# Kernel tuning notes

Measured on AMD Instinct MI355X. Metric: run time of the kernel, lower is better.

Reference implementation:

```python
import jax, jax.numpy as jnp
import numpy as np

# Physical constants and grid (match torch WRF.__init__)
PREF = 100000.0
RD = 287.0
G = 9.81
NX, NY, NZ = 384, 384, 48
DX, DY = 1000.0, 1000.0
DZ = 1.0 / (NZ + 1)

# --- staggered-grid stencil primitives (replace F.conv3d with shifts) ---

def pad_x(X):
    # periodic in x
    return jnp.concatenate([X[:, :, -1:], X, X[:, :, :1]], axis=2)

def pad_y(X):
    # periodic in y
    return jnp.concatenate([X[:, -1:, :], X, X[:, :1, :]], axis=1)

def pad_z(X, top=None, surface=None):
    # Dirichlet in z (defaults to zero boundary planes)
    top = top if top is not None else jnp.zeros_like(X[:1])
    surface = surface if surface is not None else jnp.zeros_like(X[:1])
    return jnp.concatenate([top, X, surface], axis=0)

def bar_x(X):
    return (X[:, :, 1:] + X[:, :, :-1]) * 0.5

def bar_y(X):
    return (X[:, 1:, :] + X[:, :-1, :]) * 0.5

def bar_z(X):
    return (X[1:] + X[:-1]) * 0.5

def delta_x(X):
    return (X[:, :, 1:] - X[:, :, :-1]) / DX

def delta_y(X):
    return (X[:, 1:, :] - X[:, :-1, :]) / DY

def delta_z(X):
    return (X[1:] - X[:-1]) / DZ


def rhs(U, V, W, Theta, Mu, Phi, Phi_t, Phi_s, P_t, P_s):
    u = U / bar_x(pad_x(Mu))                      # (NZ, NY, NX+1)
    v = V / bar_y(pad_y(Mu))                      # (NZ, NY+1, NX)
    w = W / bar_z(Mu)                             # (NZ-1, NY, NX)
    alpha = -delta_z(pad_z(Phi, Phi_t, Phi_s)) / Mu   # (NZ, NY, NX)
    theta = Theta / Mu
    p = PREF * (RD * theta / PREF / alpha) ** 1.4
    omega = -w * G / bar_z(alpha) / bar_z(Mu)     # (NZ-1, NY, NX)
    Omega = omega * bar_z(Mu)

    R_U = (-delta_x(bar_x(pad_x(U)) * bar_x(pad_x(u)))
           - delta_y(bar_x(pad_x(V)) * bar_y(pad_y(u)))
           - delta_z(bar_x(pad_x(pad_z(Omega))) * bar_z(pad_z(u))))
    R_V = (-delta_x(bar_y(pad_y(U)) * bar_x(pad_x(v)))
           - delta_y(bar_y(pad_y(V)) * bar_y(pad_y(v)))
           - delta_z(bar_y(pad_y(pad_z(Omega))) * bar_z(pad_z(v))))
    R_W = (-delta_x(bar_z(U) * bar_x(pad_x(w)))
           - delta_y(bar_z(V) * bar_y(pad_y(w)))
           - delta_z(bar_z(pad_z(Omega)) * bar_z(pad_z(w))))
    R_Theta = (-delta_x(U * bar_x(pad_x(theta)))
               - delta_y(V * bar_y(pad_y(theta)))
               - delta_z(pad_z(Omega) * bar_z(pad_z(theta))))
    R_Phi = (-bar_z(bar_x(u)) * delta_x(bar_x(pad_x(Phi)))
             - bar_z(bar_y(v)) * delta_y(bar_y(pad_y(Phi)))
             - omega * delta_z(bar_z(pad_z(Phi, Phi_t, Phi_s))))
    R_Mu = -delta_x(U) - delta_y(V) - delta_z(pad_z(Omega))

    # pressure-gradient terms
    R_U = R_U + (-bar_x(pad_x(Mu)) * bar_x(pad_x(alpha)) * delta_x(pad_x(p))
                 - delta_z(bar_x(bar_z(pad_x(pad_z(p, P_t, P_s)))))
                   * delta_x(pad_x(bar_z(pad_z(Phi, Phi_t, Phi_s)))))
    R_V = R_V + (-bar_y(pad_y(Mu)) * bar_y(pad_y(alpha)) * delta_y(pad_y(p))
                 - delta_z(bar_y(bar_z(pad_y(pad_z(p, P_t, P_s)))))
                   * delta_y(pad_y(bar_z(pad_z(Phi, Phi_t, Phi_s)))))
    R_W = R_W + G * (delta_z(p) - bar_z(Mu))
    R_Phi = R_Phi + G * w
    return R_U, R_V, R_W, R_Theta, R_Mu, R_Phi


def rk3_step(U, V, W, Theta, Mu, Phi, Phi_t, Phi_s, P_t, P_s, dt):
    Uc, Vc, Wc, Tc, Mc, Pc = U, V, W, Theta, Mu, Phi
    for c in (dt / 3.0, dt / 2.0, dt * 1.0):
        rU, rV, rW, rT, rM, rP = rhs(Uc, Vc, Wc, Tc, Mc, Pc, Phi_t, Phi_s, P_t, P_s)
        Uc = U + c * rU
        Vc = V + c * rV
        Wc = W + c * rW
        Tc = Theta + c * rT
        Mc = Mu + c * rM
        Pc = Phi + c * rP
    return (Uc, Vc, Wc, Tc, Mc, Pc)


def setup_inputs() -> dict:
    key = jax.random.key(0)
    k_th, k_u, k_v, k_w = jax.random.split(key, 4)
    # potential temperature with boundary layers, ~300 K
    theta_full = 300.0 + 0.5 * jax.random.normal(k_th, (NZ + 2, NY, NX), dtype=jnp.float32)
    P_t = jnp.zeros((1, NY, NX), dtype=jnp.float32)
    P_s = jnp.full((1, NY, NX), PREF, dtype=jnp.float32)
    # reproduce __init__ hydrostatic setup
    P = jnp.linspace(DZ, 1.0 - DZ, NZ, dtype=jnp.float32).reshape(NZ, 1, 1) * (P_s - P_t) + P_t
    Alpha = RD / PREF * theta_full[1:-1] * (P / PREF) ** (-1.0 / 1.4)
    Mu = jnp.broadcast_to(P_s - P_t, (NZ, NY, NX)).astype(jnp.float32)
    layer = Mu * Alpha * DZ                                  # (NZ, NY, NX)
    # Phi_full[i] = sum_{j>=i} layer[j], Phi_full[NZ] = 0
    Phi_full = jnp.concatenate(
        [jnp.flip(jnp.cumsum(jnp.flip(layer, 0), axis=0), 0),
         jnp.zeros((1, NY, NX), dtype=jnp.float32)], axis=0)  # (NZ+1, NY, NX)
    Phi_t = Phi_full[:1]
    Phi_s = Phi_full[-1:]
    Phi = Phi_full[1:-1]                                     # (NZ-1, NY, NX)
    Theta = theta_full[1:-1] * Mu
    U = 5e5 * jax.random.normal(k_u, (NZ, NY, NX + 1), dtype=jnp.float32)
    V = 5e5 * jax.random.normal(k_v, (NZ, NY + 1, NX), dtype=jnp.float32)
    W = 1e4 * jax.random.normal(k_w, (NZ - 1, NY, NX), dtype=jnp.float32)
    return {"U": U, "V": V, "W": W, "Theta": Theta, "Mu": Mu, "Phi": Phi,
            "Phi_t": Phi_t, "Phi_s": Phi_s, "P_t": P_t, "P_s": P_s, "dt": 4}


def reference(U, V, W, Theta, Mu, Phi, Phi_t, Phi_s, P_t, P_s, dt):
    return rk3_step(U, V, W, Theta, Mu, Phi, Phi_t, Phi_s, P_t, P_s, dt)
```

## Files before the change

kernel.cpp:

```cpp
#include <hip/hip_runtime.h>

namespace {

constexpr int NX = 384, NY = 384, NZ = 48;
constexpr int NXU = NX + 1;
constexpr int PLN = NX * NY;
constexpr float RDX = 1.0f / 1000.0f;
constexpr float RDY = 1.0f / 1000.0f;
constexpr float RDZ = 49.0f;
constexpr float PREF = 100000.0f, G = 9.81f;
constexpr float K_RP = 287.0f / PREF;

constexpr int SZ_U = NZ * NY * NXU;
constexpr int SZ_V = NZ * (NY + 1) * NX;
constexpr int SZ_W = (NZ - 1) * PLN;
constexpr int SZ_T = NZ * PLN;
constexpr int SZ_M = NZ * PLN;
constexpr int SZ_P = (NZ - 1) * PLN;

constexpr int TX = 32, TY = 8;
constexpr int PW = TX + 3;
constexpr int PH = TY + 3;
constexpr int PSZ = PW * PH;
constexpr int WW = PW + 1;
constexpr int WH = PH + 1;
constexpr int WSZ = WW * WH;
constexpr int ZP = 448;
constexpr int KCH = 12, KSPLIT = 4;

constexpr int O_PH = 0;
constexpr int O_MS = O_PH + 5 * ZP;
constexpr int O_UR = O_MS + 4 * ZP;
constexpr int O_VR = O_UR + 3 * ZP;
constexpr int O_TS = O_VR + 3 * ZP;
constexpr int O_WS = O_TS + ZP;
constexpr int O_P  = O_WS + ZP;
constexpr int O_OM = O_P  + 3 * PSZ;
constexpr int O_TH = O_OM + 3 * PSZ;
constexpr int O_u  = O_TH + 2 * PSZ;
constexpr int O_v  = O_u  + 2 * PSZ;
constexpr int O_w  = O_v  + 2 * PSZ;
constexpr int LTOT = O_w + 2 * PSZ;

__device__ __forceinline__ float frcp(float x) { return __builtin_amdgcn_rcpf(x); }
__device__ __forceinline__ float pow14(float x) {
    return __builtin_amdgcn_exp2f(1.4f * __builtin_amdgcn_logf(x));
}
__device__ __forceinline__ void gll4(const float* src, float* ldsWaveBase) {
    __builtin_amdgcn_global_load_lds(
        (const __attribute__((address_space(1))) void*)src,
        (__attribute__((address_space(3))) void*)ldsWaveBase, 4, 0, 0);
}
__device__ __forceinline__ int imin(int a, int b) { return a < b ? a : b; }
__device__ __forceinline__ int imax(int a, int b) { return a > b ? a : b; }

__global__ __launch_bounds__(256, 3)
void rhs_tile(
    const float* __restrict__ Us, const float* __restrict__ Vs, const float* __restrict__ Ws,
    const float* __restrict__ Ts, const float* __restrict__ Ms, const float* __restrict__ Ps,
    const float* __restrict__ Phit, const float* __restrict__ Phis,
    const float* __restrict__ Pt,   const float* __restrict__ Psrf,
    const float* __restrict__ U0, const float* __restrict__ V0, const float* __restrict__ W0,
    const float* __restrict__ T0, const float* __restrict__ M0, const float* __restrict__ P0,
    float* __restrict__ Uo, float* __restrict__ Vo, float* __restrict__ Wo,
    float* __restrict__ To, float* __restrict__ Mo, float* __restrict__ Po,
    const int* __restrict__ dtp, float coef)
{
    __shared__ float L[LTOT];

    const int tx = threadIdx.x, ty = threadIdx.y;
    const int tid = ty * TX + tx;
    const int i0 = blockIdx.x * TX;
    const int j0 = blockIdx.y * TY;
    const int k0 = blockIdx.z * KCH;
    const int i = i0 + tx, j = j0 + ty;
    const float c = coef * (float)(*dtp);
    const int ly = ty + 1, lx = tx + 1;
    const int wb = tid & ~63;
    const bool w2 = (tid < 192);
    const bool has2 = (tid + 256 < PSZ);

    auto mkcell = [&](int idx, int& pix, int& uo, int& vo) {
        const int r = idx / PW, cc = idx - r * PW;
        int gj = j0 - 1 + r;  if (gj < 0) gj += NY; else if (gj >= NY) gj -= NY;
        int gi = i0 - 1 + cc; if (gi < 0) gi += NX; else if (gi >= NX) gi -= NX;
        int gII = i0 - 1 + cc; if (gII < 0) gII += NX + 1; else if (gII > NX) gII -= NX + 1;
        int gJJ = j0 - 1 + r;  if (gJJ < 0) gJJ += NY + 1; else if (gJJ > NY) gJJ -= NY + 1;
        pix = gj * NX + gi; uo = gj * NXU + gII; vo = gJJ * NX + gi;
    };
    auto mkwide = [&](int idxw, int& pixw) {
        const int r = idxw / WW, cc = idxw - r * WW;
        int gj = j0 - 2 + r;  if (gj < 0) gj += NY; else if (gj >= NY) gj -= NY;
        int gi = i0 - 2 + cc; if (gi < 0) gi += NX; else if (gi >= NX) gi -= NX;
        pixw = gj * NX + gi;
    };
    int pixA, uoA, voA, pixB, uoB, voB, pwA, pwB;
    mkcell(tid, pixA, uoA, voA);
    mkcell(imin(tid + 256, PSZ - 1), pixB, uoB, voB);
    mkwide(tid, pwA);
    mkwide(imin(tid + 256, WSZ - 1), pwB);

    auto stage = [&](int k) {
        {
            const int m = k + 3;
            const float* sA = (m >= NZ - 1) ? &Phis[pixA] : &Ps[m * PLN + pixA];
            gll4(sA, &L[O_PH + (m % 5) * ZP + wb]);
            if (w2) {
                const float* sB = (m >= NZ - 1) ? &Phis[pixB] : &Ps[m * PLN + pixB];
                gll4(sB, &L[O_PH + (m % 5) * ZP + wb + 256]);
            }
        }
        {
            const int lc = imin(k + 3, NZ - 1);
            gll4(&Ms[lc * PLN + pwA], &L[O_MS + ((k + 3) % 4) * ZP + wb]);
            if (w2) gll4(&Ms[lc * PLN + pwB], &L[O_MS + ((k + 3) % 4) * ZP + wb + 256]);
        }
        {
            const int lc = imin(k + 2, NZ - 1);
            gll4(&Us[lc * NY * NXU + uoA], &L[O_UR + ((k + 2) % 3) * ZP + wb]);
            if (w2) gll4(&Us[lc * NY * NXU + uoB], &L[O_UR + ((k + 2) % 3) * ZP + wb + 256]);
            gll4(&Vs[lc * (NY + 1) * NX + voA], &L[O_VR + ((k + 2) % 3) * ZP + wb]);
            if (w2) gll4(&Vs[lc * (NY + 1) * NX + voB], &L[O_VR + ((k + 2) % 3) * ZP + wb + 256]);
            gll4(&Ts[lc * PLN + pixA], &L[O_TS + wb]);
            if (w2) gll4(&Ts[lc * PLN + pixB], &L[O_TS + wb + 256]);
            const int lw = imin(k + 2, NZ - 2);
            gll4(&Ws[lw * PLN + pixA], &L[O_WS + wb]);
            if (w2) gll4(&Ws[lw * PLN + pixB], &L[O_WS + wb + 256]);
        }
    };

    auto derive = [&](int l, int idx, int pix, float tsv, float wsv) {
        const int r = idx / PW, cc = idx - r * PW;
        const int wc = (r + 1) * WW + (cc + 1);
        const int s3 = ((l % 3) + 3) % 3, s2 = l & 1;
        float pv, th = 0.f, uv = 0.f, vv = 0.f, wv = 0.f, om = 0.f;
        if (l >= 0 && l < NZ) {
            const int m4 = l % 4, m5 = l % 5, p5 = ((l - 1) % 5 + 5) % 5;
            const float mu  = L[O_MS + m4 * ZP + wc];
            const float phv = L[O_PH + m5 * ZP + idx];
            const float phm = L[O_PH + p5 * ZP + idx];
            const float rmu = frcp(mu);
            const float al  = -(phv - phm) * RDZ * rmu;
            th = tsv * rmu;
            pv = PREF * pow14(K_RP * th * frcp(al));
            uv = L[O_UR + (l % 3) * ZP + idx]
                 * frcp(0.5f * (L[O_MS + m4 * ZP + wc - 1] + L[O_MS + m4 * ZP + wc]));
            vv = L[O_VR + (l % 3) * ZP + idx]
                 * frcp(0.5f * (L[O_MS + m4 * ZP + wc - WW] + L[O_MS + m4 * ZP + wc]));
            if (l < NZ - 1) {
                const float mu1 = L[O_MS + ((l + 1) % 4) * ZP + wc];
                const float ph1 = L[O_PH + ((l + 1) % 5) * ZP + idx];
                const float al1 = -(ph1 - phv) * RDZ * frcp(mu1);
                const float mz  = 0.5f * (mu + mu1);
                wv = wsv * frcp(mz);
                om = -wsv * G * frcp(0.5f * (al + al1) * mz);
            }
        } else {
            pv = (l < 0) ? Pt[pix] : Psrf[pix];
        }
        L[O_P  + s3 * PSZ + idx] = pv;
        L[O_OM + s3 * PSZ + idx] = om;
        L[O_TH + s2 * PSZ + idx] = th;
        L[O_u  + s2 * PSZ + idx] = uv;
        L[O_v  + s2 * PSZ + idx] = vv;
        L[O_w  + s2 * PSZ + idx] = wv;
    };

    {
        auto fillDirect = [&](int idx, int pix, int uo, int vo, int pixw, bool doW) {
            for (int m = k0 - 2; m <= k0 + 2; ++m) {
                float v = (m >= NZ - 1) ? Phis[pix] : ((m < 0) ? Phit[pix] : Ps[m * PLN + pix]);
                L[O_PH + ((m % 5 + 5) % 5) * ZP + idx] = v;
            }
            if (doW) {
                for (int l = k0 - 1; l <= k0 + 2; ++l) {
                    const int lc = imin(imax(l, 0), NZ - 1);
                    L[O_MS + ((l % 4 + 4) % 4) * ZP + pixw == pixw ? 0 : 0];
                }
            }
            (void)uo; (void)vo;
        };
        (void)fillDirect;
        for (int m = k0 - 2; m <= k0 + 2; ++m) {
            float v = (m >= NZ - 1) ? Phis[pixA] : ((m < 0) ? Phit[pixA] : Ps[m * PLN + pixA]);
            L[O_PH + ((m % 5 + 5) % 5) * ZP + tid] = v;
        }
        for (int l = k0 - 1; l <= k0 + 2; ++l) {
            const int lc = imin(imax(l, 0), NZ - 1);
            L[O_MS + ((l % 4 + 4) % 4) * ZP + tid] = Ms[lc * PLN + pwA];
        }
        for (int l = k0 - 1; l <= k0 + 1; ++l) {
            const int lc = imin(imax(l, 0), NZ - 1);
            L[O_UR + ((l % 3 + 3) % 3) * ZP + tid] = Us[lc * NY * NXU + uoA];
            L[O_VR + ((l % 3 + 3) % 3) * ZP + tid] = Vs[lc * (NY + 1) * NX + voA];
        }
        if (has2) {
            const int idx = tid + 256;
            for (int m = k0 - 2; m <= k0 + 2; ++m) {
                float v = (m >= NZ - 1) ? Phis[pixB] : ((m < 0) ? Phit[pixB] : Ps[m * PLN + pixB]);
                L[O_PH + ((m % 5 + 5) % 5) * ZP + idx] = v;
            }
            for (int l = k0 - 1; l <= k0 + 1; ++l) {
                const int lc = imin(imax(l, 0), NZ - 1);
                L[O_UR + ((l % 3 + 3) % 3) * ZP + idx] = Us[lc * NY * NXU + uoB];
                L[O_VR + ((l % 3 + 3) % 3) * ZP + idx] = Vs[lc * (NY + 1) * NX + voB];
            }
        }
        if (tid + 256 < WSZ) {
            const int idx = tid + 256;
            for (int l = k0 - 1; l <= k0 + 2; ++l) {
                const int lc = imin(imax(l, 0), NZ - 1);
                L[O_MS + ((l % 4 + 4) % 4) * ZP + idx] = Ms[lc * PLN + pwB];
            }
        }
    }
    __syncthreads();

    {
        int lc = imin(imax(k0 - 1, 0), NZ - 1), lw = imin(imax(k0 - 1, 0), NZ - 2);
        derive(k0 - 1, tid, pixA, Ts[lc * PLN + pixA], Ws[lw * PLN + pixA]);
        if (has2) derive(k0 - 1, tid + 256, pixB, Ts[lc * PLN + pixB], Ws[lw * PLN + pixB]);
        lc = imin(k0, NZ - 1); lw = imin(k0, NZ - 2);
        derive(k0, tid, pixA, Ts[lc * PLN + pixA], Ws[lw * PLN + pixA]);
        if (has2) derive(k0, tid + 256, pixB, Ts[lc * PLN + pixB], Ws[lw * PLN + pixB]);
    }
    {
        const int lc = imin(k0 + 1, NZ - 1), lw = imin(k0 + 1, NZ - 2);
        gll4(&Ts[lc * PLN + pixA], &L[O_TS + wb]);
        if (w2) gll4(&Ts[lc * PLN + pixB], &L[O_TS + wb + 256]);
        gll4(&Ws[lw * PLN + pixA], &L[O_WS + wb]);
        if (w2) gll4(&Ws[lw * PLN + pixB], &L[O_WS + wb + 256]);
    }
    __syncthreads();

    const int e0 = (k0 - 1) & 1;
    float th_m  = L[O_TH + e0 * PSZ + ly * PW + lx];
    float u_m   = L[O_u  + e0 * PSZ + ly * PW + lx];
    float u_m_e = L[O_u  + e0 * PSZ + ly * PW + lx + 1];
    float v_m   = L[O_v  + e0 * PSZ + (ly + 1) * PW + lx - PW + PW];
    float v_m_  = L[O_v  + e0 * PSZ + ly * PW + lx];
    float v_m_e = L[O_v  + e0 * PSZ + (ly + 1) * PW + lx];
    float w_m   = L[O_w  + e0 * PSZ + ly * PW + lx];
    v_m = v_m_;

    for (int k = k0; k < k0 + KCH; ++k) {
        derive(k + 1, tid, pixA, L[O_TS + tid], L[O_WS + tid]);
        if (has2) derive(k + 1, tid + 256, pixB, L[O_TS + tid + 256], L[O_WS + tid + 256]);
        __syncthreads();

        stage(k);

        const int a5 = (k + 4) % 5, b5 = k % 5, c5 = (k + 1) % 5;
        const int aP = (k + 2) % 3, bP = k % 3, cP = (k + 1) % 3;
        const int m4 = k % 4, n4 = (k + 1) % 4;
        const int e = k & 1, f = 1 - e;
        const int eU = k % 3, fU = (k + 1) % 3;

        auto PHx = [&](int s, int rr, int cc) { return L[O_PH + s * ZP + rr * PW + cc]; };
        auto Px  = [&](int s, int rr, int cc) { return L[O_P  + s * PSZ + rr * PW + cc]; };
        auto Ox  = [&](int s, int rr, int cc) { return L[O_OM + s * PSZ + rr * PW + cc]; };
        auto MUx = [&](int s, int rr, int cc) { return L[O_MS + s * ZP + (rr + 1) * WW + cc + 1]; };
        auto THx = [&](int s, int rr, int cc) { return L[O_TH + s * PSZ + rr * PW + cc]; };
        auto URx = [&](int s, int rr, int cc) { return L[O_UR + s * ZP + rr * PW + cc]; };
        auto VRx = [&](int s, int rr, int cc) { return L[O_VR + s * ZP + rr * PW + cc]; };
        auto ux  = [&](int s, int rr, int cc) { return L[O_u  + s * PSZ + rr * PW + cc]; };
        auto vx  = [&](int s, int rr, int cc) { return L[O_v  + s * PSZ + rr * PW + cc]; };
        auto wx  = [&](int s, int rr, int cc) { return L[O_w  + s * PSZ + rr * PW + cc]; };
        auto ALk = [&](int rr, int cc) {
            return -(PHx(b5, rr, cc) - PHx(a5, rr, cc)) * RDZ * frcp(MUx(m4, rr, cc));
        };

        auto R_U_c = [&](int cc, float ukm) -> float {
            const float u0 = ux(e, ly, cc), um = ux(e, ly, cc - 1), up = ux(e, ly, cc + 1);
            const float Uc = URx(eU, ly, cc), Um = URx(eU, ly, cc - 1), Up = URx(eU, ly, cc + 1);
            float r = -0.25f * ((Uc + Up) * (u0 + up) - (Um + Uc) * (um + u0)) * RDX;
            const float VBj  = 0.5f * (VRx(eU, ly, cc - 1) + VRx(eU, ly, cc));
            const float VBj1 = 0.5f * (VRx(eU, ly + 1, cc - 1) + VRx(eU, ly + 1, cc));
            const float uS = ux(e, ly - 1, cc), uN = ux(e, ly + 1, cc);
            r -= (VBj1 * 0.5f * (u0 + uN) - VBj * 0.5f * (uS + u0)) * RDY;
            const float OBk  = 0.5f * (Ox(aP, ly, cc - 1) + Ox(aP, ly, cc));
            const float OBk1 = 0.5f * (Ox(bP, ly, cc - 1) + Ox(bP, ly, cc));
            const float ukp = ux(f, ly, cc);
            r -= (OBk1 * 0.5f * (u0 + ukp) - OBk * 0.5f * (ukm + u0)) * RDZ;
            const float mux_ = 0.5f * (MUx(m4, ly, cc - 1) + MUx(m4, ly, cc));
            const float alx  = 0.5f * (ALk(ly, cc - 1) + ALk(ly, cc));
            const float dpx  = (Px(bP, ly, cc) - Px(bP, ly, cc - 1)) * RDX;
            r -= mux_ * alx * dpx;
            const float pzk  = 0.25f * (Px(aP, ly, cc - 1) + Px(bP, ly, cc - 1)
                                      + Px(aP, ly, cc)     + Px(bP, ly, cc));
            const float pzk1 = 0.25f * (Px(bP, ly, cc - 1) + Px(cP, ly, cc - 1)
                                      + Px(bP, ly, cc)     + Px(cP, ly, cc));
            const float dpz = (pzk1 - pzk) * RDZ;
            const float pza = 0.5f * (PHx(a5, ly, cc - 1) + PHx(b5, ly, cc - 1));
            const float pzb = 0.5f * (PHx(a5, ly, cc)     + PHx(b5, ly, cc));
            r -= dpz * (pzb - pza) * RDX;
            return r;
        };

        auto R_V_c = [&](int rr, float vkm) -> float {
            const float v0 = vx(e, rr, lx), vm = vx(e, rr - 1, lx), vp = vx(e, rr + 1, lx);
            const float Vc = VRx(eU, rr, lx), Vm = VRx(eU, rr - 1, lx), Vp = VRx(eU, rr + 1, lx);
            float r = -0.25f * ((Vc + Vp) * (v0 + vp) - (Vm + Vc) * (vm + v0)) * RDY;
            const float UBi  = 0.5f * (URx(eU, rr - 1, lx)     + URx(eU, rr, lx));
            const float UBi1 = 0.5f * (URx(eU, rr - 1, lx + 1) + URx(eU, rr, lx + 1));
            const float vW = vx(e, rr, lx - 1), vE = vx(e, rr, lx + 1);
            r -= (UBi1 * 0.5f * (v0 + vE) - UBi * 0.5f * (vW + v0)) * RDX;
            const float OBk  = 0.5f * (Ox(aP, rr - 1, lx) + Ox(aP, rr, lx));
            const float OBk1 = 0.5f * (Ox(bP, rr - 1, lx) + Ox(bP, rr, lx));
            const float vkp = vx(f, rr, lx);
            r -= (OBk1 * 0.5f * (v0 + vkp) - OBk * 0.5f * (vkm + v0)) * RDZ;
            const float muy = 0.5f * (MUx(m4, rr - 1, lx) + MUx(m4, rr, lx));
            const float aly = 0.5f * (ALk(rr - 1, lx) + ALk(rr, lx));
            const float dpy = (Px(bP, rr, lx) - Px(bP, rr - 1, lx)) * RDY;
            r -= muy * aly * dpy;
            const float pzk  = 0.25f * (Px(aP, rr - 1, lx) + Px(bP, rr - 1, lx)
                                      + Px(aP, rr, lx)     + Px(bP, rr, lx));
            const float pzk1 = 0.25f * (Px(bP, rr - 1, lx) + Px(cP, rr - 1, lx)
                                      + Px(bP, rr, lx)     + Px(cP, rr, lx));
            const float dpz = (pzk1 - pzk) * RDZ;
            const float pza = 0.5f * (PHx(a5, rr - 1, lx) + PHx(b5, rr - 1, lx));
            const float pzb = 0.5f * (PHx(a5, rr, lx)     + PHx(b5, rr, lx));
            r -= dpz * (pzb - pza) * RDY;
            return r;
        };

        const float th0 = THx(e, ly, lx);
        float rT = -(URx(eU, ly, lx + 1) * 0.5f * (th0 + THx(e, ly, lx + 1))
                   - URx(eU, ly, lx)     * 0.5f * (THx(e, ly, lx - 1) + th0)) * RDX
                   -(VRx(eU, ly + 1, lx) * 0.5f * (th0 + THx(e, ly + 1, lx))
                   - VRx(eU, ly, lx)     * 0.5f * (THx(e, ly - 1, lx) + th0)) * RDY;
        const float th_p = THx(f, ly, lx);
        const float Hk  = Ox(aP, ly, lx) * 0.5f * (th_m + th0);
        const float Hk1 = Ox(bP, ly, lx) * 0.5f * (th0 + th_p);
        rT -= (Hk1 - Hk) * RDZ;

        const float rM = -(URx(eU, ly, lx + 1) - URx(eU, ly, lx)) * RDX
                         -(VRx(eU, ly + 1, lx) - VRx(eU, ly, lx)) * RDY
                         -(Ox(bP, ly, lx) - Ox(aP, ly, lx)) * RDZ;

        const int idc = (k * NY + j) * NX + i;
        To[idc] = T0[idc] + c * rT;
        Mo[idc] = M0[idc] + c * rM;
        const int idu = (k * NY + j) * NXU + i;
        Uo[idu] = U0[idu] + c * R_U_c(lx, u_m);
        const int idv = (k * (NY + 1) + j) * NX + i;
        Vo[idv] = V0[idv] + c * R_V_c(ly, v_m);

        if (k < NZ - 1) {
            const float w0 = wx(e, ly, lx);
            const float Uzi  = 0.5f * (URx(eU, ly, lx)     + URx(fU, ly, lx));
            const float Uzi1 = 0.5f * (URx(eU, ly, lx + 1) + URx(fU, ly, lx + 1));
            const float wW = wx(e, ly, lx - 1), wE = wx(e, ly, lx + 1);
            float rW = -(Uzi1 * 0.5f * (w0 + wE) - Uzi * 0.5f * (wW + w0)) * RDX;
            const float Vzj  = 0.5f * (VRx(eU, ly, lx)     + VRx(fU, ly, lx));
            const float Vzj1 = 0.5f * (VRx(eU, ly + 1, lx) + VRx(fU, ly + 1, lx));
            const float wS = wx(e, ly - 1, lx), wN = wx(e, ly + 1, lx);
            rW -= (Vzj1 * 0.5f * (w0 + wN) - Vzj * 0.5f * (wS + w0)) * RDY;
            const float OZk  = 0.5f * (Ox(aP, ly, lx) + Ox(bP, ly, lx));
            const float OZk1 = 0.5f * (Ox(bP, ly, lx) + Ox(cP, ly, lx));
            const float wkp = wx(f, ly, lx);
            rW -= (OZk1 * 0.5f * (w0 + wkp) - OZk * 0.5f * (w_m + w0)) * RDZ;
            const float muz = 0.5f * (MUx(m4, ly, lx) + MUx(n4, ly, lx));
            rW += G * ((Px(cP, ly, lx) - Px(bP, ly, lx)) * RDZ - muz);

            const float ubz = 0.25f * (ux(e, ly, lx) + ux(e, ly, lx + 1)
                                     + ux(f, ly, lx) + ux(f, ly, lx + 1));
            const float dfx = (PHx(b5, ly, lx + 1) - PHx(b5, ly, lx - 1)) * (0.5f * RDX);
            const float vbz = 0.25f * (vx(e, ly, lx) + vx(e, ly + 1, lx)
                                     + vx(f, ly, lx) + vx(f, ly + 1, lx));
            const float dfy = (PHx(b5, ly + 1, lx) - PHx(b5, ly - 1, lx)) * (0.5f * RDY);
            const float rmuz = frcp(muz);
            const float om   = Ox(bP, ly, lx) * rmuz;
            const float dfz  = (PHx(c5, ly, lx) - PHx(a5, ly, lx)) * (0.5f * RDZ);
            const float rP = -ubz * dfx - vbz * dfy - om * dfz + G * w0;

            Wo[idc] = W0[idc] + c * rW;
            Po[idc] = P0[idc] + c * rP;
        }

        if (i == NX - 1) {
            Uo[idu + 1] = U0[idu + 1] + c * R_U_c(lx + 1, u_m_e);
        }
        if (j == NY - 1) {
            const int idv2 = (k * (NY + 1) + NY) * NX + i;
            Vo[idv2] = V0[idv2] + c * R_V_c(ly + 1, v_m_e);
        }

        th_m  = th0;
        u_m   = ux(e, ly, lx);
        u_m_e = ux(e, ly, lx + 1);
        v_m   = vx(e, ly, lx);
        v_m_e = vx(e, ly + 1, lx);
        w_m   = wx(e, ly, lx);

        __syncthreads();
    }
}

}

extern "C" void kernel_launch(void* const* d_in, const int* in_sizes, int n_in,
                              void* d_out, int out_size, void* d_ws, size_t ws_size,
                              hipStream_t stream)
{
    (void)in_sizes; (void)n_in; (void)out_size; (void)ws_size;

    const float* U0   = (const float*)d_in[0];
    const float* V0   = (const float*)d_in[1];
    const float* W0   = (const float*)d_in[2];
    const float* T0   = (const float*)d_in[3];
    const float* M0   = (const float*)d_in[4];
    const float* P0   = (const float*)d_in[5];
    const float* Phit = (const float*)d_in[6];
    const float* Phis = (const float*)d_in[7];
    const float* Pt   = (const float*)d_in[8];
    const float* Psrf = (const float*)d_in[9];
    const int*   dtp  = (const int*)d_in[10];

    float* out = (float*)d_out;
    float* ws  = (float*)d_ws;

    float* outU = out;
    float* outV = outU + SZ_U;
    float* outW = outV + SZ_V;
    float* outT = outW + SZ_W;
    float* outM = outT + SZ_T;
    float* outP = outM + SZ_M;

    float* wsU = ws;
    float* wsV = wsU + SZ_U;
    float* wsW = wsV + SZ_V;
    float* wsT = wsW + SZ_W;
    float* wsM = wsT + SZ_T;
    float* wsP = wsM + SZ_M;

    const dim3 blk(TX, TY, 1);
    const dim3 grd(NX / TX, NY / TY, KSPLIT);

    const float coefs[3] = {1.0f / 3.0f, 0.5f, 1.0f};

    const float* sU[3] = {U0, outU, wsU};
    const float* sV[3] = {V0, outV, wsV};
    const float* sW[3] = {W0, outW, wsW};
    const float* sT[3] = {T0, outT, wsT};
    const float* sM[3] = {M0, outM, wsM};
    const float* sP_[3] = {P0, outP, wsP};
    float* oU[3] = {outU, wsU, outU};
    float* oV[3] = {outV, wsV, outV};
    float* oW[3] = {outW, wsW, outW};
    float* oT[3] = {outT, wsT, outT};
    float* oM[3] = {outM, wsM, outM};
    float* oP[3] = {outP, wsP, outP};

    for (int s = 0; s < 3; ++s) {
        rhs_tile<<<grd, blk, 0, stream>>>(
            sU[s], sV[s], sW[s], sT[s], sM[s], sP_[s],
            Phit, Phis, Pt, Psrf,
            U0, V0, W0, T0, M0, P0,
            oU[s], oV[s], oW[s], oT[s], oM[s], oP[s],
            dtp, coefs[s]);
    }
}
```

Measured before the change: 606.8 us.

## Switch to 16x16 tiles with a one-cell halo and tighter LDS layout

Changes the thread tile from 32x8 to 16x16 and shrinks the halo from 3 to 2 cells, so the LDS footprint per block drops and occupancy is raised to 4 blocks per CU. Halo cells past the async-load range are staged with scalar loads in a tail path, and the east/north edge faces now fetch the wrapped U/V value directly from global memory instead of relying on the wider halo. The aim is less redundant halo traffic and more resident waves. The cost is more boundary special-casing, extra scalar loads, and a square tile that may coalesce less well along x.

After: 715.6 us. 1.18x slower.

```diff
diff --git a/kernel.cpp b/kernel.cpp
--- a/kernel.cpp
+++ b/kernel.cpp
@@ -18,29 +18,29 @@
 constexpr int SZ_M = NZ * PLN;
 constexpr int SZ_P = (NZ - 1) * PLN;
 
-constexpr int TX = 32, TY = 8;
-constexpr int PW = TX + 3;
-constexpr int PH = TY + 3;
+constexpr int TX = 16, TY = 16;
+constexpr int PW = TX + 2;
+constexpr int PH = TY + 2;
 constexpr int PSZ = PW * PH;
 constexpr int WW = PW + 1;
-constexpr int WH = PH + 1;
-constexpr int WSZ = WW * WH;
-constexpr int ZP = 448;
+constexpr int WSZ = WW * WW;
 constexpr int KCH = 12, KSPLIT = 4;
 
 constexpr int O_PH = 0;
-constexpr int O_MS = O_PH + 5 * ZP;
-constexpr int O_UR = O_MS + 4 * ZP;
-constexpr int O_VR = O_UR + 3 * ZP;
-constexpr int O_TS = O_VR + 3 * ZP;
-constexpr int O_WS = O_TS + ZP;
-constexpr int O_P  = O_WS + ZP;
+constexpr int O_MS = O_PH + 5 * PSZ;
+constexpr int O_UR = O_MS + 4 * WSZ;
+constexpr int O_VR = O_UR + 3 * PSZ;
+constexpr int O_TS = O_VR + 3 * PSZ;
+constexpr int O_WS = O_TS + PSZ;
+constexpr int O_P  = O_WS + PSZ;
 constexpr int O_OM = O_P  + 3 * PSZ;
 constexpr int O_TH = O_OM + 3 * PSZ;
 constexpr int O_u  = O_TH + 2 * PSZ;
 constexpr int O_v  = O_u  + 2 * PSZ;
 constexpr int O_w  = O_v  + 2 * PSZ;
 constexpr int LTOT = O_w + 2 * PSZ;
+
+struct PIdx { int pix, uo, vo, wc, oxa, oxb, oya, oyb; };
 
 __device__ __forceinline__ float frcp(float x) { return __builtin_amdgcn_rcpf(x); }
 __device__ __forceinline__ float pow14(float x) {
@@ -54,7 +54,7 @@
 __device__ __forceinline__ int imin(int a, int b) { return a < b ? a : b; }
 __device__ __forceinline__ int imax(int a, int b) { return a > b ? a : b; }
 
-__global__ __launch_bounds__(256, 3)
+__global__ __launch_bounds__(256, 4)
 void rhs_tile(
     const float* __restrict__ Us, const float* __restrict__ Vs, const float* __restrict__ Ws,
     const float* __restrict__ Ts, const float* __restrict__ Ms, const float* __restrict__ Ps,
@@ -77,86 +77,118 @@
     const float c = coef * (float)(*dtp);
     const int ly = ty + 1, lx = tx + 1;
     const int wb = tid & ~63;
-    const bool w2 = (tid < 192);
-    const bool has2 = (tid + 256 < PSZ);
-
-    auto mkcell = [&](int idx, int& pix, int& uo, int& vo) {
+    const bool hasB = (tid + 256 < PSZ);
+    const bool hasW = (tid + 256 < WSZ);
+
+    auto mkpt = [&](int idx, PIdx& q) {
         const int r = idx / PW, cc = idx - r * PW;
         int gj = j0 - 1 + r;  if (gj < 0) gj += NY; else if (gj >= NY) gj -= NY;
         int gi = i0 - 1 + cc; if (gi < 0) gi += NX; else if (gi >= NX) gi -= NX;
-        int gII = i0 - 1 + cc; if (gII < 0) gII += NX + 1; else if (gII > NX) gII -= NX + 1;
-        int gJJ = j0 - 1 + r;  if (gJJ < 0) gJJ += NY + 1; else if (gJJ > NY) gJJ -= NY + 1;
-        pix = gj * NX + gi; uo = gj * NXU + gII; vo = gJJ * NX + gi;
+        int gII = i0 - 1 + cc; if (gII < 0) gII += NX + 1;
+        int gJJ = j0 - 1 + r;  if (gJJ < 0) gJJ += NY + 1;
+        q.pix = gj * NX + gi;
+        q.uo  = gj * NXU + gII;
+        q.vo  = gJJ * NX + gi;
+        q.wc  = (r + 1) * WW + (cc + 1);
+        q.oxa = q.wc - 1; q.oxb = q.wc;
+        if (i0 == 0 && cc == 0) { q.oxa = q.wc; q.oxb = q.wc + 1; }
+        q.oya = q.wc - WW; q.oyb = q.wc;
+        if (j0 == 0 && r == 0)  { q.oya = q.wc; q.oyb = q.wc + WW; }
     };
-    auto mkwide = [&](int idxw, int& pixw) {
+    auto mkwide = [&](int idxw) -> int {
         const int r = idxw / WW, cc = idxw - r * WW;
         int gj = j0 - 2 + r;  if (gj < 0) gj += NY; else if (gj >= NY) gj -= NY;
         int gi = i0 - 2 + cc; if (gi < 0) gi += NX; else if (gi >= NX) gi -= NX;
-        pixw = gj * NX + gi;
+        return gj * NX + gi;
     };
-    int pixA, uoA, voA, pixB, uoB, voB, pwA, pwB;
-    mkcell(tid, pixA, uoA, voA);
-    mkcell(imin(tid + 256, PSZ - 1), pixB, uoB, voB);
-    mkwide(tid, pwA);
-    mkwide(imin(tid + 256, WSZ - 1), pwB);
+    PIdx A, B;
+    mkpt(tid, A);
+    mkpt(imin(tid + 256, PSZ - 1), B);
+    const int pwA = mkwide(tid);
+    const int pwB = mkwide(imin(tid + 256, WSZ - 1));
+
+    const int tpi = tid - 64;
+    const bool hasTail  = (tpi >= 0 && tpi < PSZ - 320);
+    const int twi = tid - 68;
+    const bool hasWTail = (twi >= 0 && twi < WSZ - 320);
+    PIdx Tq;
+    mkpt(hasTail ? (320 + tpi) : 0, Tq);
+    const int pwT = mkwide(hasWTail ? (320 + twi) : 0);
 
     auto stage = [&](int k) {
         {
             const int m = k + 3;
-            const float* sA = (m >= NZ - 1) ? &Phis[pixA] : &Ps[m * PLN + pixA];
-            gll4(sA, &L[O_PH + (m % 5) * ZP + wb]);
-            if (w2) {
-                const float* sB = (m >= NZ - 1) ? &Phis[pixB] : &Ps[m * PLN + pixB];
-                gll4(sB, &L[O_PH + (m % 5) * ZP + wb + 256]);
+            const float* sA = (m >= NZ - 1) ? &Phis[A.pix] : &Ps[m * PLN + A.pix];
+            gll4(sA, &L[O_PH + (m % 5) * PSZ + wb]);
+            if (tid < 64) {
+                const float* sB = (m >= NZ - 1) ? &Phis[B.pix] : &Ps[m * PLN + B.pix];
+                gll4(sB, &L[O_PH + (m % 5) * PSZ + wb + 256]);
             }
         }
         {
-            const int lc = imin(k + 3, NZ - 1);
-            gll4(&Ms[lc * PLN + pwA], &L[O_MS + ((k + 3) % 4) * ZP + wb]);
-            if (w2) gll4(&Ms[lc * PLN + pwB], &L[O_MS + ((k + 3) % 4) * ZP + wb + 256]);
+            const int lm = imin(k + 3, NZ - 1);
+            gll4(&Ms[lm * PLN + pwA], &L[O_MS + ((k + 3) % 4) * WSZ + wb]);
+            if (tid < 64) gll4(&Ms[lm * PLN + pwB], &L[O_MS + ((k + 3) % 4) * WSZ + wb + 256]);
         }
         {
             const int lc = imin(k + 2, NZ - 1);
-            gll4(&Us[lc * NY * NXU + uoA], &L[O_UR + ((k + 2) % 3) * ZP + wb]);
-            if (w2) gll4(&Us[lc * NY * NXU + uoB], &L[O_UR + ((k + 2) % 3) * ZP + wb + 256]);
-            gll4(&Vs[lc * (NY + 1) * NX + voA], &L[O_VR + ((k + 2) % 3) * ZP + wb]);
-            if (w2) gll4(&Vs[lc * (NY + 1) * NX + voB], &L[O_VR + ((k + 2) % 3) * ZP + wb + 256]);
-            gll4(&Ts[lc * PLN + pixA], &L[O_TS + wb]);
-            if (w2) gll4(&Ts[lc * PLN + pixB], &L[O_TS + wb + 256]);
+            gll4(&Us[lc * NY * NXU + A.uo], &L[O_UR + ((k + 2) % 3) * PSZ + wb]);
+            if (tid < 64) gll4(&Us[lc * NY * NXU + B.uo], &L[O_UR + ((k + 2) % 3) * PSZ + wb + 256]);
+            gll4(&Vs[lc * (NY + 1) * NX + A.vo], &L[O_VR + ((k + 2) % 3) * PSZ + wb]);
+            if (tid < 64) gll4(&Vs[lc * (NY + 1) * NX + B.vo], &L[O_VR + ((k + 2) % 3) * PSZ + wb + 256]);
+            gll4(&Ts[lc * PLN + A.pix], &L[O_TS + wb]);
+            if (tid < 64) gll4(&Ts[lc * PLN + B.pix], &L[O_TS + wb + 256]);
             const int lw = imin(k + 2, NZ - 2);
-            gll4(&Ws[lw * PLN + pixA], &L[O_WS + wb]);
-            if (w2) gll4(&Ws[lw * PLN + pixB], &L[O_WS + wb + 256]);
+            gll4(&Ws[lw * PLN + A.pix], &L[O_WS + wb]);
+            if (tid < 64) gll4(&Ws[lw * PLN + B.pix], &L[O_WS + wb + 256]);
         }
     };
 
-    auto derive = [&](int l, int idx, int pix, float tsv, float wsv) {
-        const int r = idx / PW, cc = idx - r * PW;
-        const int wc = (r + 1) * WW + (cc + 1);
+    auto stage_tail = [&](int k) {
+        if (hasTail) {
+            const int idx = 320 + tpi;
+            const int m = k + 3;
+            L[O_PH + (m % 5) * PSZ + idx] =
+                (m >= NZ - 1) ? Phis[Tq.pix] : Ps[m * PLN + Tq.pix];
+            const int lc = imin(k + 2, NZ - 1);
+            L[O_UR + ((k + 2) % 3) * PSZ + idx] = Us[lc * NY * NXU + Tq.uo];
+            L[O_VR + ((k + 2) % 3) * PSZ + idx] = Vs[lc * (NY + 1) * NX + Tq.vo];
+            L[O_TS + idx] = Ts[lc * PLN + Tq.pix];
+            const int lw = imin(k + 2, NZ - 2);
+            L[O_WS + idx] = Ws[lw * PLN + Tq.pix];
+        }
+        if (hasWTail) {
+            const int lm = imin(k + 3, NZ - 1);
+            L[O_MS + ((k + 3) % 4) * WSZ + 320 + twi] = Ms[lm * PLN + pwT];
+        }
+    };
+
+    auto derive = [&](int l, int idx, const PIdx& q, float tsv, float wsv) {
         const int s3 = ((l % 3) + 3) % 3, s2 = l & 1;
         float pv, th = 0.f, uv = 0.f, vv = 0.f, wv = 0.f, om = 0.f;
         if (l >= 0 && l < NZ) {
             const int m4 = l % 4, m5 = l % 5, p5 = ((l - 1) % 5 + 5) % 5;
-            const float mu  = L[O_MS + m4 * ZP + wc];
-            const float phv = L[O_PH + m5 * ZP + idx];
-            const float phm = L[O_PH + p5 * ZP + idx];
+            const float mu  = L[O_MS + m4 * WSZ + q.wc];
+            const float phv = L[O_PH + m5 * PSZ + idx];
+            const float phm = L[O_PH + p5 * PSZ + idx];
             const float rmu = frcp(mu);
             const float al  = -(phv - phm) * RDZ * rmu;
             th = tsv * rmu;
             pv = PREF * pow14(K_RP * th * frcp(al));
-            uv = L[O_UR + (l % 3) * ZP + idx]
-                 * frcp(0.5f * (L[O_MS + m4 * ZP + wc - 1] + L[O_MS + m4 * ZP + wc]));
-            vv = L[O_VR + (l % 3) * ZP + idx]
-                 * frcp(0.5f * (L[O_MS + m4 * ZP + wc - WW] + L[O_MS + m4 * ZP + wc]));
+            uv = L[O_UR + (l % 3) * PSZ + idx]
+                 * frcp(0.5f * (L[O_MS + m4 * WSZ + q.oxa] + L[O_MS + m4 * WSZ + q.oxb]));
+            vv = L[O_VR + (l % 3) * PSZ + idx]
+                 * frcp(0.5f * (L[O_MS + m4 * WSZ + q.oya] + L[O_MS + m4 * WSZ + q.oyb]));
             if (l < NZ - 1) {
-                const float mu1 = L[O_MS + ((l + 1) % 4) * ZP + wc];
-                const float ph1 = L[O_PH + ((l + 1) % 5) * ZP + idx];
+                const float mu1 = L[O_MS + ((l + 1) % 4) * WSZ + q.wc];
+                const float ph1 = L[O_PH + ((l + 1) % 5) * PSZ + idx];
                 const float al1 = -(ph1 - phv) * RDZ * frcp(mu1);
                 const float mz  = 0.5f * (mu + mu1);
                 wv = wsv * frcp(mz);
                 om = -wsv * G * frcp(0.5f * (al + al1) * mz);
             }
         } else {
-            pv = (l < 0) ? Pt[pix] : Psrf[pix];
+            pv = (l < 0) ? Pt[q.pix] : Psrf[q.pix];
         }
         L[O_P  + s3 * PSZ + idx] = pv;
         L[O_OM + s3 * PSZ + idx] = om;
@@ -167,50 +199,38 @@
     };
 
     {
-        auto fillDirect = [&](int idx, int pix, int uo, int vo, int pixw, bool doW) {
-            for (int m = k0 - 2; m <= k0 + 2; ++m) {
-                float v = (m >= NZ - 1) ? Phis[pix] : ((m < 0) ? Phit[pix] : Ps[m * PLN + pix]);
-                L[O_PH + ((m % 5 + 5) % 5) * ZP + idx] = v;
-            }
-            if (doW) {
-                for (int l = k0 - 1; l <= k0 + 2; ++l) {
-                    const int lc = imin(imax(l, 0), NZ - 1);
-                    L[O_MS + ((l % 4 + 4) % 4) * ZP + pixw == pixw ? 0 : 0];
-                }
-            }
-            (void)uo; (void)vo;
-        };
-        (void)fillDirect;
         for (int m = k0 - 2; m <= k0 + 2; ++m) {
-            float v = (m >= NZ - 1) ? Phis[pixA] : ((m < 0) ? Phit[pixA] : Ps[m * PLN + pixA]);
-            L[O_PH + ((m % 5 + 5) % 5) * ZP + tid] = v;
+            const float v = (m >= NZ - 1) ? Phis[A.pix]
+                          : ((m < 0) ? Phit[A.pix] : Ps[m * PLN + A.pix]);
+            L[O_PH + ((m % 5 + 5) % 5) * PSZ + tid] = v;
         }
         for (int l = k0 - 1; l <= k0 + 2; ++l) {
             const int lc = imin(imax(l, 0), NZ - 1);
-            L[O_MS + ((l % 4 + 4) % 4) * ZP + tid] = Ms[lc * PLN + pwA];
+            L[O_MS + ((l % 4 + 4) % 4) * WSZ + tid] = Ms[lc * PLN + pwA];
         }
         for (int l = k0 - 1; l <= k0 + 1; ++l) {
             const int lc = imin(imax(l, 0), NZ - 1);
-            L[O_UR + ((l % 3 + 3) % 3) * ZP + tid] = Us[lc * NY * NXU + uoA];
-            L[O_VR + ((l % 3 + 3) % 3) * ZP + tid] = Vs[lc * (NY + 1) * NX + voA];
-        }
-        if (has2) {
+            L[O_UR + ((l % 3 + 3) % 3) * PSZ + tid] = Us[lc * NY * NXU + A.uo];
+            L[O_VR + ((l % 3 + 3) % 3) * PSZ + tid] = Vs[lc * (NY + 1) * NX + A.vo];
+        }
+        if (hasB) {
             const int idx = tid + 256;
             for (int m = k0 - 2; m <= k0 + 2; ++m) {
-                float v = (m >= NZ - 1) ? Phis[pixB] : ((m < 0) ? Phit[pixB] : Ps[m * PLN + pixB]);
-                L[O_PH + ((m % 5 + 5) % 5) * ZP + idx] = v;
+                const float v = (m >= NZ - 1) ? Phis[B.pix]
+                              : ((m < 0) ? Phit[B.pix] : Ps[m * PLN + B.pix]);
+                L[O_PH + ((m % 5 + 5) % 5) * PSZ + idx] = v;
             }
             for (int l = k0 - 1; l <= k0 + 1; ++l) {
                 const int lc = imin(imax(l, 0), NZ - 1);
-                L[O_UR + ((l % 3 + 3) % 3) * ZP + idx] = Us[lc * NY * NXU + uoB];
-                L[O_VR + ((l % 3 + 3) % 3) * ZP + idx] = Vs[lc * (NY + 1) * NX + voB];
+                L[O_UR + ((l % 3 + 3) % 3) * PSZ + idx] = Us[lc * NY * NXU + B.uo];
+                L[O_VR + ((l % 3 + 3) % 3) * PSZ + idx] = Vs[lc * (NY + 1) * NX + B.vo];
             }
         }
-        if (tid + 256 < WSZ) {
+        if (hasW) {
             const int idx = tid + 256;
             for (int l = k0 - 1; l <= k0 + 2; ++l) {
                 const int lc = imin(imax(l, 0), NZ - 1);
-                L[O_MS + ((l % 4 + 4) % 4) * ZP + idx] = Ms[lc * PLN + pwB];
+                L[O_MS + ((l % 4 + 4) % 4) * WSZ + idx] = Ms[lc * PLN + pwB];
             }
         }
     }
@@ -218,18 +238,22 @@
 
     {
         int lc = imin(imax(k0 - 1, 0), NZ - 1), lw = imin(imax(k0 - 1, 0), NZ - 2);
-        derive(k0 - 1, tid, pixA, Ts[lc * PLN + pixA], Ws[lw * PLN + pixA]);
-        if (has2) derive(k0 - 1, tid + 256, pixB, Ts[lc * PLN + pixB], Ws[lw * PLN + pixB]);
+        derive(k0 - 1, tid, A, Ts[lc * PLN + A.pix], Ws[lw * PLN + A.pix]);
+        if (hasB) derive(k0 - 1, tid + 256, B, Ts[lc * PLN + B.pix], Ws[lw * PLN + B.pix]);
         lc = imin(k0, NZ - 1); lw = imin(k0, NZ - 2);
-        derive(k0, tid, pixA, Ts[lc * PLN + pixA], Ws[lw * PLN + pixA]);
-        if (has2) derive(k0, tid + 256, pixB, Ts[lc * PLN + pixB], Ws[lw * PLN + pixB]);
+        derive(k0, tid, A, Ts[lc * PLN + A.pix], Ws[lw * PLN + A.pix]);
+        if (hasB) derive(k0, tid + 256, B, Ts[lc * PLN + B.pix], Ws[lw * PLN + B.pix]);
     }
     {
         const int lc = imin(k0 + 1, NZ - 1), lw = imin(k0 + 1, NZ - 2);
-        gll4(&Ts[lc * PLN + pixA], &L[O_TS + wb]);
-        if (w2) gll4(&Ts[lc * PLN + pixB], &L[O_TS + wb + 256]);
-        gll4(&Ws[lw * PLN + pixA], &L[O_WS + wb]);
-        if (w2) gll4(&Ws[lw * PLN + pixB], &L[O_WS + wb + 256]);
+        gll4(&Ts[lc * PLN + A.pix], &L[O_TS + wb]);
+        if (tid < 64) gll4(&Ts[lc * PLN + B.pix], &L[O_TS + wb + 256]);
+        gll4(&Ws[lw * PLN + A.pix], &L[O_WS + wb]);
+        if (tid < 64) gll4(&Ws[lw * PLN + B.pix], &L[O_WS + wb + 256]);
+        if (hasTail) {
+            L[O_TS + 320 + tpi] = Ts[lc * PLN + Tq.pix];
+            L[O_WS + 320 + tpi] = Ws[lw * PLN + Tq.pix];
+        }
     }
     __syncthreads();
 
@@ -237,15 +261,14 @@
     float th_m  = L[O_TH + e0 * PSZ + ly * PW + lx];
     float u_m   = L[O_u  + e0 * PSZ + ly * PW + lx];
     float u_m_e = L[O_u  + e0 * PSZ + ly * PW + lx + 1];
-    float v_m   = L[O_v  + e0 * PSZ + (ly + 1) * PW + lx - PW + PW];
-    float v_m_  = L[O_v  + e0 * PSZ + ly * PW + lx];
+    float v_m   = L[O_v  + e0 * PSZ + ly * PW + lx];
     float v_m_e = L[O_v  + e0 * PSZ + (ly + 1) * PW + lx];
     float w_m   = L[O_w  + e0 * PSZ + ly * PW + lx];
-    v_m = v_m_;
 
     for (int k = k0; k < k0 + KCH; ++k) {
-        derive(k + 1, tid, pixA, L[O_TS + tid], L[O_WS + tid]);
-        if (has2) derive(k + 1, tid + 256, pixB, L[O_TS + tid + 256], L[O_WS + tid + 256]);
+        derive(k + 1, tid, A, L[O_TS + tid], L[O_WS + tid]);
+        if (hasB) derive(k + 1, tid + 256, B, L[O_TS + tid + 256], L[O_WS + tid + 256]);
+        stage_tail(k);
         __syncthreads();
 
         stage(k);
@@ -256,13 +279,13 @@
         const int e = k & 1, f = 1 - e;
         const int eU = k % 3, fU = (k + 1) % 3;
 
-        auto PHx = [&](int s, int rr, int cc) { return L[O_PH + s * ZP + rr * PW + cc]; };
+        auto PHx = [&](int s, int rr, int cc) { return L[O_PH + s * PSZ + rr * PW + cc]; };
         auto Px  = [&](int s, int rr, int cc) { return L[O_P  + s * PSZ + rr * PW + cc]; };
         auto Ox  = [&](int s, int rr, int cc) { return L[O_OM + s * PSZ + rr * PW + cc]; };
-        auto MUx = [&](int s, int rr, int cc) { return L[O_MS + s * ZP + (rr + 1) * WW + cc + 1]; };
+        auto MUx = [&](int s, int rr, int cc) { return L[O_MS + s * WSZ + (rr + 1) * WW + cc + 1]; };
         auto THx = [&](int s, int rr, int cc) { return L[O_TH + s * PSZ + rr * PW + cc]; };
-        auto URx = [&](int s, int rr, int cc) { return L[O_UR + s * ZP + rr * PW + cc]; };
-        auto VRx = [&](int s, int rr, int cc) { return L[O_VR + s * ZP + rr * PW + cc]; };
+        auto URx = [&](int s, int rr, int cc) { return L[O_UR + s * PSZ + rr * PW + cc]; };
+        auto VRx = [&](int s, int rr, int cc) { return L[O_VR + s * PSZ + rr * PW + cc]; };
         auto ux  = [&](int s, int rr, int cc) { return L[O_u  + s * PSZ + rr * PW + cc]; };
         auto vx  = [&](int s, int rr, int cc) { return L[O_v  + s * PSZ + rr * PW + cc]; };
         auto wx  = [&](int s, int rr, int cc) { return L[O_w  + s * PSZ + rr * PW + cc]; };
@@ -270,9 +293,12 @@
             return -(PHx(b5, rr, cc) - PHx(a5, rr, cc)) * RDZ * frcp(MUx(m4, rr, cc));
         };
 
-        auto R_U_c = [&](int cc, float ukm) -> float {
-            const float u0 = ux(e, ly, cc), um = ux(e, ly, cc - 1), up = ux(e, ly, cc + 1);
-            const float Uc = URx(eU, ly, cc), Um = URx(eU, ly, cc - 1), Up = URx(eU, ly, cc + 1);
+        auto R_U_c = [&](int cc, float ukm, float Upov, bool edge) -> float {
+            const float u0 = ux(e, ly, cc), um = ux(e, ly, cc - 1);
+            const float up = edge ? Upov * frcp(0.5f * (MUx(m4, ly, PW - 2) + MUx(m4, ly, PW - 1)))
+                                  : ux(e, ly, cc + 1);
+            const float Uc = URx(eU, ly, cc), Um = URx(eU, ly, cc - 1);
+            const float Up = edge ? Upov : URx(eU, ly, cc + 1);
             float r = -0.25f * ((Uc + Up) * (u0 + up) - (Um + Uc) * (um + u0)) * RDX;
             const float VBj  = 0.5f * (VRx(eU, ly, cc - 1) + VRx(eU, ly, cc));
             const float VBj1 = 0.5f * (VRx(eU, ly + 1, cc - 1) + VRx(eU, ly + 1, cc));
@@ -297,9 +323,12 @@
             return r;
         };
 
-        auto R_V_c = [&](int rr, float vkm) -> float {
-            const float v0 = vx(e, rr, lx), vm = vx(e, rr - 1, lx), vp = vx(e, rr + 1, lx);
-            const float Vc = VRx(eU, rr, lx), Vm = VRx(eU, rr - 1, lx), Vp = VRx(eU, rr + 1, lx);
+        auto R_V_c = [&](int rr, float vkm, float Vpov, bool edge) -> float {
+            const float v0 = vx(e, rr, lx), vm = vx(e, rr - 1, lx);
+            const float vp = edge ? Vpov * frcp(0.5f * (MUx(m4, PH - 2, lx) + MUx(m4, PH - 1, lx)))
+                                  : vx(e, rr + 1, lx);
+            const float Vc = VRx(eU, rr, lx), Vm = VRx(eU, rr - 1, lx);
+            const float Vp = edge ? Vpov : VRx(eU, rr + 1, lx);
             float r = -0.25f * ((Vc + Vp) * (v0 + vp) - (Vm + Vc) * (vm + v0)) * RDY;
             const float UBi  = 0.5f * (URx(eU, rr - 1, lx)     + URx(eU, rr, lx));
             const float UBi1 = 0.5f * (URx(eU, rr - 1, lx + 1) + URx(eU, rr, lx + 1));
@@ -342,9 +371,9 @@
         To[idc] = T0[idc] + c * rT;
         Mo[idc] = M0[idc] + c * rM;
         const int idu = (k * NY + j) * NXU + i;
-        Uo[idu] = U0[idu] + c * R_U_c(lx, u_m);
+        Uo[idu] = U0[idu] + c * R_U_c(lx, u_m, 0.0f, false);
         const int idv = (k * (NY + 1) + j) * NX + i;
-        Vo[idv] = V0[idv] + c * R_V_c(ly, v_m);
+        Vo[idv] = V0[idv] + c * R_V_c(ly, v_m, 0.0f, false);
 
         if (k < NZ - 1) {
             const float w0 = wx(e, ly, lx);
@@ -379,11 +408,13 @@
         }
 
         if (i == NX - 1) {
-            Uo[idu + 1] = U0[idu + 1] + c * R_U_c(lx + 1, u_m_e);
+            const float Ug = Us[k * NY * NXU + j * NXU];
+            Uo[idu + 1] = U0[idu + 1] + c * R_U_c(lx + 1, u_m_e, Ug, true);
         }
         if (j == NY - 1) {
+            const float Vg = Vs[k * (NY + 1) * NX + i];
             const int idv2 = (k * (NY + 1) + NY) * NX + i;
-            Vo[idv2] = V0[idv2] + c * R_V_c(ly + 1, v_m_e);
+            Vo[idv2] = V0[idv2] + c * R_V_c(ly + 1, v_m_e, Vg, true);
         }
 
         th_m  = th0;
```
